# Optimization experiments

Hardware: AMD Instinct MI355X
Metric: run time of the kernel (lower is better)

Reference implementation:

```python
import jax, jax.numpy as jnp
import numpy as np

K_ATTRS = 16  # fixed number of attribute clusters (torch.unique made static for jit)
NEG_INF = jnp.float32(-1e9)


def setup_inputs() -> dict:
    key = jax.random.key(0)
    ks = jax.random.split(key, 20)
    B, T, V, D, H = 4096, 200, 100000, 64, 64
    M0, M1 = 256, 128
    FC_IN = D + D + H + D  # 256
    s = 0.02
    f32 = jnp.float32
    inp = {
        "item_id": jax.random.randint(ks[0], (B,), 0, V),
        "hist_item_ids": jax.random.randint(ks[1], (B, T), 0, V),
        "hist_item_attributes": jax.random.randint(ks[2], (B, T), 0, K_ATTRS),
        "emb_table": s * jax.random.normal(ks[3], (V, D), dtype=f32),
        "au_W1": s * jax.random.normal(ks[4], (4 * D, H), dtype=f32),
        "au_b1": jnp.zeros((H,), f32),
        "au_W2": s * jax.random.normal(ks[5], (H, 1), dtype=f32),
        "au_b2": jnp.zeros((1,), f32),
        "gru_Wx": s * jax.random.normal(ks[6], (D, 3 * H), dtype=f32),
        "gru_Wh": s * jax.random.normal(ks[7], (H, 3 * H), dtype=f32),
        "gru_b": jnp.zeros((3 * H,), f32),
        "fc_W0": s * jax.random.normal(ks[8], (FC_IN, M0), dtype=f32),
        "fc_b0": jnp.zeros((M0,), f32),
        "fc_W1": s * jax.random.normal(ks[9], (M0, M1), dtype=f32),
        "fc_b1": jnp.zeros((M1,), f32),
        "final_W": s * jax.random.normal(ks[10], (M1, 1), dtype=f32),
        "final_b": jnp.zeros((1,), f32),
    }
    return inp


def reference(item_id, hist_item_ids, hist_item_attributes, emb_table,
              au_W1, au_b1, au_W2, au_b2, gru_Wx, gru_Wh, gru_b,
              fc_W0, fc_b0, fc_W1, fc_b1, final_W, final_b):
    item = emb_table[item_id]            # [B,D]
    hist = emb_table[hist_item_ids]      # [B,T,D]
    B = item.shape[0]
    H = gru_Wh.shape[0]

    # --- DIEN: GRU over history, final hidden state ---
    xp = hist @ gru_Wx + gru_b           # [B,T,3H]

    def step(h, x):
        gz, gr, gn = jnp.split(h @ gru_Wh, 3, axis=-1)
        xz, xr, xn = jnp.split(x, 3, axis=-1)
        z = jax.nn.sigmoid(xz + gz)
        r = jax.nn.sigmoid(xr + gr)
        n = jnp.tanh(xn + r * gn)
        return (1.0 - z) * n + z * h, None

    h0 = jnp.zeros((B, H), hist.dtype)
    interest_evolution, _ = jax.lax.scan(step, h0, jnp.swapaxes(xp, 0, 1))  # [B,H]

    # --- DIN-style activation unit: score each key against the target item ---
    def act_unit(q, keys):  # q:[B,D], keys:[B,N,D] -> [B,N,1]
        qe = jnp.broadcast_to(q[:, None, :], keys.shape)
        feat = jnp.concatenate([keys, qe, keys - qe, keys * qe], axis=-1)
        hid = jax.nn.relu(feat @ au_W1 + au_b1)
        return hid @ au_W2 + au_b2

    w1 = act_unit(item, hist)                    # [B,T,1]
    user_interest_l1 = jnp.sum(w1 * hist, axis=1)  # [B,D]

    # --- attribute_group: per-attribute masked softmax + weighted sum ---
    mask = hist_item_attributes[..., None] == jnp.arange(K_ATTRS)  # [B,T,K]
    logits = jnp.where(mask, w1, NEG_INF)        # [B,T,K]
    probs = jax.nn.softmax(logits, axis=1) * mask
    cluster = jnp.einsum('btk,btd->bkd', probs, hist)  # [B,K,D]

    w2 = act_unit(item, cluster)                 # [B,K,1]
    user_interest_l2 = jnp.sum(w2 * cluster, axis=1)  # [B,D]

    combined = jnp.concatenate(
        [user_interest_l1, user_interest_l2, interest_evolution, item], axis=1)
    x = jax.nn.relu(combined @ fc_W0 + fc_b0)
    x = jax.nn.relu(x @ fc_W1 + fc_b1)
    out = x @ final_W + final_b                  # [B,1]
    return jax.nn.sigmoid(out[:, 0])             # [B]
```

## Files before the change

### kernel.cpp

```cpp
#include <hip/hip_runtime.h>
#include <hip/hip_bf16.h>

#define B_   4096
#define T_   200
#define KA   16

#define OFF_BG  0
#define OFF_WQ  4096
#define OFF_QP  (OFF_BG  + B_*T_)
#define OFF_UI1 (OFF_QP  + B_*64)
#define OFF_UI2 (OFF_UI1 + B_*64)
#define OFF_HF  (OFF_UI2 + B_*64)
#define OFF_CL  (OFF_HF  + B_*64)

typedef __attribute__((ext_vector_type(8))) short bf16x8;
typedef __attribute__((ext_vector_type(4))) float f32x4;

__device__ __forceinline__ float sigmoidf_(float x) {
  return 1.f / (1.f + __expf(-x));
}
__device__ __forceinline__ float sigf(float x) {
  return __builtin_amdgcn_rcpf(1.f + __builtin_amdgcn_exp2f(-1.44269504f * x));
}
__device__ __forceinline__ float tanhfast(float y) {
  return 1.f - 2.f * __builtin_amdgcn_rcpf(1.f + __builtin_amdgcn_exp2f(2.88539008f * y));
}
__device__ __forceinline__ short f2bf(float x) {
  unsigned u = __float_as_uint(x);
  unsigned r = (u + 0x7fffu + ((u >> 16) & 1u)) >> 16;
  return (short)r;
}
__device__ __forceinline__ unsigned cvtpk(float lo, float hi) {
  unsigned r;
  asm("v_cvt_pk_bf16_f32 %0, %1, %2" : "=v"(r) : "v"(lo), "v"(hi));
  return r;
}
union BF8 { bf16x8 v; unsigned u[4]; };

__device__ __forceinline__ bf16x8 pack8(float4 f0, float4 f1) {
  BF8 a;
  a.u[0] = cvtpk(f0.x, f0.y);
  a.u[1] = cvtpk(f0.z, f0.w);
  a.u[2] = cvtpk(f1.x, f1.y);
  a.u[3] = cvtpk(f1.z, f1.w);
  return a.v;
}
__device__ __forceinline__ bf16x8 pack8m(float4 f0, float4 f1,
                                         float4 q0, float4 q1) {
  BF8 a;
  a.u[0] = cvtpk(f0.x*q0.x, f0.y*q0.y);
  a.u[1] = cvtpk(f0.z*q0.z, f0.w*q0.w);
  a.u[2] = cvtpk(f1.x*q1.x, f1.y*q1.y);
  a.u[3] = cvtpk(f1.z*q1.z, f1.w*q1.w);
  return a.v;
}


__global__ __launch_bounds__(256) void k_prep(
    const float* __restrict__ auW1, short* __restrict__ bg,
    float* __restrict__ wq)
{
  const int i = blockIdx.x*256 + threadIdx.x;
  if (i < 8192) {
    const int k = i >> 6, col = i & 63;
    float v;
    if (k < 64) v = auW1[k*64 + col] + auW1[2*4096 + k*64 + col];
    else        v = auW1[3*4096 + (k-64)*64 + col];
    bg[((k >> 5)*4 + ((k >> 3) & 3))*512 + col*8 + (k & 7)] = f2bf(v);
  } else if (i < 12288) {
    const int j = i - 8192;
    wq[j] = auW1[(64 + (j >> 6))*64 + (j & 63)]
          - auW1[(128 + (j >> 6))*64 + (j & 63)];
  }
}

__global__ __launch_bounds__(256) void k_act1(
    const int* __restrict__ item_id, const int* __restrict__ hist_ids,
    const int* __restrict__ attrs,
    const float* __restrict__ emb, const float* __restrict__ aub1,
    const float* __restrict__ auW2, const float* __restrict__ aub2,
    const short* __restrict__ bg_in, const float* __restrict__ wq_in,
    float* __restrict__ qp_out, float* __restrict__ ui1_out,
    float* __restrict__ cluster_out)
{
  __shared__ __align__(16) char sPool[16384];
  __shared__ float sW1[208];
  __shared__ float sP[200];
  __shared__ float sM[KA], sE[KA];
  __shared__ float sItem[64], sQp[64];
  __shared__ float sQpP[4][64];
  __shared__ float sUi[4][64];
  __shared__ int   sIds[200], sAttr[200];

  short* sB2 = (short*)sPool;
  float (*sAcc)[KA][64] = (float (*)[KA][64])sPool;

  const int b = blockIdx.x;
  const int tid = threadIdx.x;
  const int wave = tid >> 6, lane = tid & 63;
  const int g = lane >> 4;
  const int c15 = lane & 15;
  const int itrow = item_id[b];

  for (int i = tid; i < 4096; i += 256)
    ((unsigned*)sB2)[i] = ((const unsigned*)bg_in)[i];
  if (tid < 64) sItem[tid] = emb[(size_t)itrow*64 + tid];
  if (tid < T_) {
    sIds[tid]  = hist_ids[(size_t)b*T_ + tid];
    sAttr[tid] = attrs[(size_t)b*T_ + tid];
  }
  __syncthreads();

  {
    const int j = tid & 63, iq = tid >> 6;
    float acc = 0.f;
    #pragma unroll
    for (int ii = 0; ii < 16; ++ii) {
      const int i = iq*16 + ii;
      acc += sItem[i] * wq_in[i*64 + j];
    }
    sQpP[iq][j] = acc;
  }
  __syncthreads();
  if (tid < 64) {
    float q = aub1[tid] + sQpP[0][tid] + sQpP[1][tid] + sQpP[2][tid] + sQpP[3][tid];
    sQp[tid] = q;
    qp_out[(size_t)b*64 + tid] = q;
  }
  __syncthreads();

  const float4* itemp = (const float4*)(emb + (size_t)itrow*64);
  float4 q0 = itemp[g*2],     q1 = itemp[g*2 + 1];
  float4 q2 = itemp[8 + g*2], q3 = itemp[8 + g*2 + 1];

  bf16x8 bfr[4][4];
  #pragma unroll
  for (int kk = 0; kk < 4; ++kk) {
    #pragma unroll
    for (int n = 0; n < 4; ++n)
      bfr[kk][n] = *(const bf16x8*)&sB2[(kk*4 + g)*512 + (n*16 + c15)*8];
  }
  float w2v[4], qpv[4];
  #pragma unroll
  for (int n = 0; n < 4; ++n) {
    w2v[n] = auW2[n*16 + c15];
    qpv[n] = sQp[n*16 + c15];
  }
  const float b2v = aub2[0];
  __syncthreads();

  for (int i = tid; i < 4*KA*64; i += 256) ((float*)sAcc)[i] = 0.f;

  for (int tt = wave; tt < 13; tt += 4) {
    const int t = tt*16 + c15;
    float4 k0{0,0,0,0}, k1{0,0,0,0}, k2{0,0,0,0}, k3{0,0,0,0};
    if (t < T_) {
      const float4* kp = (const float4*)(emb + (size_t)sIds[t]*64);
      k0 = kp[g*2];     k1 = kp[g*2 + 1];
      k2 = kp[8 + g*2]; k3 = kp[8 + g*2 + 1];
    }
    bf16x8 a0 = pack8(k0, k1);
    bf16x8 a1 = pack8(k2, k3);
    bf16x8 a2 = pack8m(k0, k1, q0, q1);
    bf16x8 a3 = pack8m(k2, k3, q2, q3);

    f32x4 acc[4];
    #pragma unroll
    for (int n = 0; n < 4; ++n) acc[n] = f32x4{qpv[n], qpv[n], qpv[n], qpv[n]};
    #pragma unroll
    for (int n = 0; n < 4; ++n) {
      acc[n] = __builtin_amdgcn_mfma_f32_16x16x32_bf16(a0, bfr[0][n], acc[n], 0, 0, 0);
      acc[n] = __builtin_amdgcn_mfma_f32_16x16x32_bf16(a1, bfr[1][n], acc[n], 0, 0, 0);
      acc[n] = __builtin_amdgcn_mfma_f32_16x16x32_bf16(a2, bfr[2][n], acc[n], 0, 0, 0);
      acc[n] = __builtin_amdgcn_mfma_f32_16x16x32_bf16(a3, bfr[3][n], acc[n], 0, 0, 0);
    }
    float ws[4] = {0.f, 0.f, 0.f, 0.f};
    #pragma unroll
    for (int n = 0; n < 4; ++n) {
      #pragma unroll
      for (int r = 0; r < 4; ++r)
        ws[r] += fmaxf(acc[n][r], 0.f) * w2v[n];
    }
    #pragma unroll
    for (int r = 0; r < 4; ++r) {
      ws[r] += __shfl_xor(ws[r], 1);
      ws[r] += __shfl_xor(ws[r], 2);
      ws[r] += __shfl_xor(ws[r], 4);
      ws[r] += __shfl_xor(ws[r], 8);
      ws[r] += b2v;
    }
    if (c15 == 0) {
      #pragma unroll
      for (int r = 0; r < 4; ++r) {
        const int trow = tt*16 + g*4 + r;
        if (trow < T_) sW1[trow] = ws[r];
      }
    }
  }
  __syncthreads();

  for (int k = wave; k < KA; k += 4) {
    float m = -1e9f;
    for (int tt4 = 0; tt4 < 4; ++tt4) {
      int t = tt4*64 + lane;
      if (t < T_ && sAttr[t] == k) m = fmaxf(m, sW1[t]);
    }
    #pragma unroll
    for (int off = 32; off > 0; off >>= 1) m = fmaxf(m, __shfl_xor(m, off));
    float e = 0.f;
    for (int tt4 = 0; tt4 < 4; ++tt4) {
      int t = tt4*64 + lane;
      if (t < T_ && sAttr[t] == k) e += __expf(sW1[t] - m);
    }
    #pragma unroll
    for (int off = 32; off > 0; off >>= 1) e += __shfl_xor(e, off);
    if (lane == 0) { sM[k] = m; sE[k] = e; }
  }
  __syncthreads();
  if (tid < T_) {
    int k = sAttr[tid];
    float e = sE[k];
    sP[tid] = (e > 0.f) ? __expf(sW1[tid] - sM[k]) * __builtin_amdgcn_rcpf(e) : 0.f;
  }
  __syncthreads();

  float uiacc = 0.f;
  {
    float vcur = emb[(size_t)sIds[wave]*64 + lane];
    for (int t = wave; t < T_; t += 4) {
      const int tn = t + 4;
      float vnext = 0.f;
      if (tn < T_) vnext = emb[(size_t)sIds[tn]*64 + lane];
      const int k = sAttr[t];
      sAcc[wave][k][lane] += sP[t] * vcur;
      uiacc += sW1[t] * vcur;
      vcur = vnext;
    }
  }
  sUi[wave][lane] = uiacc;
  __syncthreads();

  for (int i = tid; i < KA*64; i += 256) {
    cluster_out[(size_t)b*(KA*64) + i] =
        sAcc[0][0][i] + sAcc[1][0][i] + sAcc[2][0][i] + sAcc[3][0][i];
  }
  if (tid < 64) {
    ui1_out[(size_t)b*64 + tid] =
        sUi[0][tid] + sUi[1][tid] + sUi[2][tid] + sUi[3][tid];
  }
}

#define GRU_ROWS 16
__global__ __launch_bounds__(512) void k_gru(
    const int* __restrict__ hist_ids, const float* __restrict__ emb,
    const float* __restrict__ Wx, const float* __restrict__ Wh,
    const float* __restrict__ gb, float* __restrict__ hfin_out)
{
  __shared__ short sH[2][16*64];
  __shared__ short sX[4][16*64];
  __shared__ int   sIds[16*200];

  const int tid  = threadIdx.x;
  const int w    = tid >> 6;
  const int lane = tid & 63;
  const int g    = lane >> 4;
  const int c15  = lane & 15;
  const int b0   = blockIdx.x * GRU_ROWS;

  for (int i = tid; i < 16*200; i += 512) {
    const int r = i / 200, t = i - r*200;
    sIds[i] = hist_ids[(size_t)(b0 + r)*T_ + t];
  }
  for (int i = tid; i < 16*64; i += 512) sH[0][i] = 0;
  __syncthreads();

  if (w >= 4) {
    const int stane = (w - 4)*64 + lane;
    const int srow  = stane >> 4;
    const int scol  = (stane & 15) * 4;
    const int sidx  = srow*64 + (((scol >> 3) ^ (srow & 7))*8) + (scol & 7);
    const int* idrow = &sIds[srow*200];
    #pragma unroll
    for (int p = 0; p < 2; ++p) {
      const float4 f = *(const float4*)(emb + (size_t)idrow[p]*64 + scol);
      uint2 u; u.x = cvtpk(f.x, f.y); u.y = cvtpk(f.z, f.w);
      *(uint2*)&sX[p][sidx] = u;
    }
    __syncthreads();
    for (int t = 0; t < T_; ++t) {
      const int t2 = (t + 2 < T_) ? (t + 2) : (T_ - 1);
      const float4 f = *(const float4*)(emb + (size_t)idrow[t2]*64 + scol);
      uint2 u; u.x = cvtpk(f.x, f.y); u.y = cvtpk(f.z, f.w);
      *(uint2*)&sX[(t + 2) & 3][sidx] = u;
      __syncthreads();
    }
  } else {
    bf16x8 bx[3][2], bh[3][2];
    #pragma unroll
    for (int l = 0; l < 3; ++l) {
      const int jb = (l*4 + w)*16 + c15;
      #pragma unroll
      for (int kk = 0; kk < 2; ++kk) {
        bf16x8 vx, vh;
        #pragma unroll
        for (int e = 0; e < 8; ++e) {
          const int krow = kk*32 + g*8 + e;
          vx[e] = f2bf(Wx[(size_t)krow*192 + jb]);
          vh[e] = f2bf(Wh[(size_t)krow*192 + jb]);
        }
        bx[l][kk] = vx; bh[l][kk] = vh;
      }
    }
    float bias[3];
    #pragma unroll
    for (int l = 0; l < 3; ++l) bias[l] = gb[l*64 + w*16 + c15];

    const int rs = c15 & 7;
    const int ridx0 = c15*64 + ((g    ) ^ rs)*8;
    const int ridx1 = c15*64 + ((g + 4) ^ rs)*8;
    int widx[4];
    {
      const int unit = w*2 + (c15 >> 3);
      #pragma unroll
      for (int r = 0; r < 4; ++r) {
        const int row = g*4 + r;
        widx[r] = row*64 + ((unit ^ (row & 7))*8) + (c15 & 7);
      }
    }
    float hold[4] = {0.f, 0.f, 0.f, 0.f};
    __syncthreads();

    #pragma unroll 2
    for (int t = 0; t < T_; ++t) {
      const short* hbuf = sH[t & 1];
      short*       hnxt = sH[(t & 1) ^ 1];
      const short* xbuf = sX[t & 3];

      bf16x8 ax0 = *(const bf16x8*)&xbuf[ridx0];
      bf16x8 ax1 = *(const bf16x8*)&xbuf[ridx1];
      bf16x8 ah0 = *(const bf16x8*)&hbuf[ridx0];
      bf16x8 ah1 = *(const bf16x8*)&hbuf[ridx1];

      f32x4 aX[3], aH[3];
      #pragma unroll
      for (int l = 0; l < 3; ++l) {
        aX[l] = f32x4{bias[l], bias[l], bias[l], bias[l]};
        aH[l] = f32x4{0.f, 0.f, 0.f, 0.f};
      }
      #pragma unroll
      for (int l = 0; l < 3; ++l) {
        aH[l] = __builtin_amdgcn_mfma_f32_16x16x32_bf16(ah0, bh[l][0], aH[l], 0, 0, 0);
        aH[l] = __builtin_amdgcn_mfma_f32_16x16x32_bf16(ah1, bh[l][1], aH[l], 0, 0, 0);
        aX[l] = __builtin_amdgcn_mfma_f32_16x16x32_bf16(ax0, bx[l][0], aX[l], 0, 0, 0);
        aX[l] = __builtin_amdgcn_mfma_f32_16x16x32_bf16(ax1, bx[l][1], aX[l], 0, 0, 0);
      }

      #pragma unroll
      for (int r = 0; r < 4; ++r) {
        float z  = sigf(aX[0][r] + aH[0][r]);
        float rr = sigf(aX[1][r] + aH[1][r]);
        float nn = tanhfast(aX[2][r] + rr * aH[2][r]);
        hold[r] = nn + z * (hold[r] - nn);
        hnxt[widx[r]] = f2bf(hold[r]);
      }
      __syncthreads();
    }

    #pragma unroll
    for (int r = 0; r < 4; ++r)
      hfin_out[(size_t)(b0 + g*4 + r)*64 + w*16 + c15] = hold[r];
  }
}

__global__ __launch_bounds__(256) void k_act2(
    const int* __restrict__ item_id, const float* __restrict__ emb,
    const float* __restrict__ auW2, const float* __restrict__ aub2,
    const float* __restrict__ qp_in, const float* __restrict__ cluster_in,
    const short* __restrict__ bg_in, float* __restrict__ ui2_out)
{
  __shared__ short sB2[8192];
  __shared__ float sWs[4][16];
  __shared__ float sWf[16];
  __shared__ float sUi[4][64];

  const int b = blockIdx.x;
  const int tid = threadIdx.x;
  const int wave = tid >> 6, lane = tid & 63;
  const int g = lane >> 4;
  const int c15 = lane & 15;
  const int itrow = item_id[b];

  for (int i = tid; i < 4096; i += 256)
    ((unsigned*)sB2)[i] = ((const unsigned*)bg_in)[i];
  __syncthreads();

  const float4* itemp = (const float4*)(emb + (size_t)itrow*64);
  float4 q0 = itemp[g*2],     q1 = itemp[g*2 + 1];
  float4 q2 = itemp[8 + g*2], q3 = itemp[8 + g*2 + 1];
  const float4* kp = (const float4*)(cluster_in + (size_t)b*(KA*64) + c15*64);
  float4 k0 = kp[g*2],     k1 = kp[g*2 + 1];
  float4 k2 = kp[8 + g*2], k3 = kp[8 + g*2 + 1];
  bf16x8 a0 = pack8(k0, k1);
  bf16x8 a1 = pack8(k2, k3);
  bf16x8 a2 = pack8m(k0, k1, q0, q1);
  bf16x8 a3 = pack8m(k2, k3, q2, q3);

  const float qpv = qp_in[(size_t)b*64 + wave*16 + c15];
  const float w2v = auW2[wave*16 + c15];
  f32x4 acc = f32x4{qpv, qpv, qpv, qpv};
  acc = __builtin_amdgcn_mfma_f32_16x16x32_bf16(a0, *(const bf16x8*)&sB2[(0*4+g)*512 + (wave*16+c15)*8], acc, 0, 0, 0);
  acc = __builtin_amdgcn_mfma_f32_16x16x32_bf16(a1, *(const bf16x8*)&sB2[(1*4+g)*512 + (wave*16+c15)*8], acc, 0, 0, 0);
  acc = __builtin_amdgcn_mfma_f32_16x16x32_bf16(a2, *(const bf16x8*)&sB2[(2*4+g)*512 + (wave*16+c15)*8], acc, 0, 0, 0);
  acc = __builtin_amdgcn_mfma_f32_16x16x32_bf16(a3, *(const bf16x8*)&sB2[(3*4+g)*512 + (wave*16+c15)*8], acc, 0, 0, 0);

  float ws[4];
  #pragma unroll
  for (int r = 0; r < 4; ++r) {
    float v = fmaxf(acc[r], 0.f) * w2v;
    v += __shfl_xor(v, 1);
    v += __shfl_xor(v, 2);
    v += __shfl_xor(v, 4);
    v += __shfl_xor(v, 8);
    ws[r] = v;
  }
  if (c15 == 0) {
    #pragma unroll
    for (int r = 0; r < 4; ++r) sWs[wave][g*4 + r] = ws[r];
  }
  __syncthreads();
  if (tid < KA)
    sWf[tid] = sWs[0][tid] + sWs[1][tid] + sWs[2][tid] + sWs[3][tid] + aub2[0];
  __syncthreads();

  float uiacc = 0.f;
  #pragma unroll
  for (int kk = 0; kk < 4; ++kk) {
    const int k = wave*4 + kk;
    uiacc += sWf[k] * cluster_in[(size_t)b*(KA*64) + k*64 + lane];
  }
  sUi[wave][lane] = uiacc;
  __syncthreads();
  if (tid < 64) {
    ui2_out[(size_t)b*64 + tid] =
        sUi[0][tid] + sUi[1][tid] + sUi[2][tid] + sUi[3][tid];
  }
}

#define MLP_ROWS 16
__global__ __launch_bounds__(256) void k_mlp(
    const int* __restrict__ item_id, const float* __restrict__ emb,
    const float* __restrict__ ui1, const float* __restrict__ ui2,
    const float* __restrict__ hfin,
    const float* __restrict__ W0, const float* __restrict__ b0,
    const float* __restrict__ W1, const float* __restrict__ b1,
    const float* __restrict__ fW, const float* __restrict__ fb,
    float* __restrict__ out)
{
  __shared__ float sC[MLP_ROWS][256];
  __shared__ float sX0[MLP_ROWS][256];
  __shared__ float sX1[MLP_ROWS][128];
  const int tid = threadIdx.x;
  const int rb  = blockIdx.x * MLP_ROWS;

  for (int idx = tid; idx < MLP_ROWS*256; idx += 256) {
    int r = idx >> 8, c = idx & 255;
    size_t row = (size_t)(rb + r);
    float v;
    if (c < 64)       v = ui1[row*64 + c];
    else if (c < 128) v = ui2[row*64 + (c-64)];
    else if (c < 192) v = hfin[row*64 + (c-128)];
    else              v = emb[(size_t)item_id[row]*64 + (c-192)];
    sC[r][c] = v;
  }
  __syncthreads();
  {
    float acc[MLP_ROWS];
    #pragma unroll
    for (int r = 0; r < MLP_ROWS; ++r) acc[r] = b0[tid];
    #pragma unroll 4
    for (int i = 0; i < 256; ++i) {
      float w = W0[(size_t)i*256 + tid];
      #pragma unroll
      for (int r = 0; r < MLP_ROWS; ++r) acc[r] += sC[r][i] * w;
    }
    #pragma unroll
    for (int r = 0; r < MLP_ROWS; ++r) sX0[r][tid] = fmaxf(acc[r], 0.f);
  }
  __syncthreads();
  if (tid < 128) {
    float acc[MLP_ROWS];
    #pragma unroll
    for (int r = 0; r < MLP_ROWS; ++r) acc[r] = b1[tid];
    #pragma unroll 4
    for (int i = 0; i < 256; ++i) {
      float w = W1[(size_t)i*128 + tid];
      #pragma unroll
      for (int r = 0; r < MLP_ROWS; ++r) acc[r] += sX0[r][i] * w;
    }
    #pragma unroll
    for (int r = 0; r < MLP_ROWS; ++r) sX1[r][tid] = fmaxf(acc[r], 0.f);
  }
  __syncthreads();
  {
    int r = tid >> 4, l16 = tid & 15;
    float p = 0.f;
    for (int i = l16; i < 128; i += 16) p += sX1[r][i] * fW[i];
    #pragma unroll
    for (int off = 8; off > 0; off >>= 1) p += __shfl_xor(p, off);
    if (l16 == 0) {
      float logit = p + fb[0];
      out[rb + r] = sigmoidf_(logit);
    }
  }
}

extern "C" void kernel_launch(void* const* d_in, const int* in_sizes, int n_in,
                              void* d_out, int out_size, void* d_ws, size_t ws_size,
                              hipStream_t stream)
{
  const int*   item_id  = (const int*)d_in[0];
  const int*   hist_ids = (const int*)d_in[1];
  const int*   attrs    = (const int*)d_in[2];
  const float* emb      = (const float*)d_in[3];
  const float* auW1     = (const float*)d_in[4];
  const float* aub1     = (const float*)d_in[5];
  const float* auW2     = (const float*)d_in[6];
  const float* aub2     = (const float*)d_in[7];
  const float* gWx      = (const float*)d_in[8];
  const float* gWh      = (const float*)d_in[9];
  const float* gb       = (const float*)d_in[10];
  const float* W0       = (const float*)d_in[11];
  const float* b0       = (const float*)d_in[12];
  const float* W1       = (const float*)d_in[13];
  const float* b1       = (const float*)d_in[14];
  const float* fW       = (const float*)d_in[15];
  const float* fb       = (const float*)d_in[16];

  float* out = (float*)d_out;
  float* ws  = (float*)d_ws;
  short* bg      = (short*)(ws + OFF_BG);
  float* wq      = ws + OFF_WQ;
  float* qp      = ws + OFF_QP;
  float* ui1     = ws + OFF_UI1;
  float* ui2     = ws + OFF_UI2;
  float* hfin    = ws + OFF_HF;
  float* cluster = ws + OFF_CL;

  k_prep<<<48, 256, 0, stream>>>(auW1, bg, wq);
  k_act1<<<B_, 256, 0, stream>>>(item_id, hist_ids, attrs, emb, aub1,
                                 auW2, aub2, bg, wq, qp, ui1, cluster);
  k_gru<<<B_/GRU_ROWS, 512, 0, stream>>>(hist_ids, emb, gWx, gWh, gb, hfin);
  k_act2<<<B_, 256, 0, stream>>>(item_id, emb, auW2, aub2, qp, cluster, bg,
                                 ui2);
  k_mlp<<<B_/MLP_ROWS, 256, 0, stream>>>(item_id, emb, ui1, ui2, hfin,
                                         W0, b0, W1, b1, fW, fb, out);
}
```

Before: 324.6 us.

## Stage bf16 history rows in LDS and compute cluster sums from them

The act1 kernel now writes the bf16-packed history embeddings into a swizzled LDS buffer during the MFMA scoring pass. It then reuses that buffer for the per-attribute cluster sums and the l1 interest sum, replacing a second global gather of the fp32 embeddings. Each wave now owns four attribute clusters in registers instead of doing shared-memory atomic-like accumulation plus a 4-way reduction. The scoring loop also prefetches the next tile's rows. The trade-off is bf16 precision for the weighted sums, and each wave now loops over all 200 timesteps.

After: 408.7 us. 25.9% more time.

```diff
diff --git a/kernel.cpp b/kernel.cpp
--- a/kernel.cpp
+++ b/kernel.cpp
@@ -29,6 +29,9 @@
   unsigned u = __float_as_uint(x);
   unsigned r = (u + 0x7fffu + ((u >> 16) & 1u)) >> 16;
   return (short)r;
+}
+__device__ __forceinline__ float bf2f(unsigned short h) {
+  return __uint_as_float((unsigned)h << 16);
 }
 __device__ __forceinline__ unsigned cvtpk(float lo, float hi) {
   unsigned r;
@@ -83,7 +86,7 @@
     float* __restrict__ qp_out, float* __restrict__ ui1_out,
     float* __restrict__ cluster_out)
 {
-  __shared__ __align__(16) char sPool[16384];
+  __shared__ __align__(16) short sKp[13*1024];
   __shared__ float sW1[208];
   __shared__ float sP[200];
   __shared__ float sM[KA], sE[KA];
@@ -92,9 +95,6 @@
   __shared__ float sUi[4][64];
   __shared__ int   sIds[200], sAttr[200];
 
-  short* sB2 = (short*)sPool;
-  float (*sAcc)[KA][64] = (float (*)[KA][64])sPool;
-
   const int b = blockIdx.x;
   const int tid = threadIdx.x;
   const int wave = tid >> 6, lane = tid & 63;
@@ -103,7 +103,7 @@
   const int itrow = item_id[b];
 
   for (int i = tid; i < 4096; i += 256)
-    ((unsigned*)sB2)[i] = ((const unsigned*)bg_in)[i];
+    ((unsigned*)sKp)[i] = ((const unsigned*)bg_in)[i];
   if (tid < 64) sItem[tid] = emb[(size_t)itrow*64 + tid];
   if (tid < T_) {
     sIds[tid]  = hist_ids[(size_t)b*T_ + tid];
@@ -138,7 +138,7 @@
   for (int kk = 0; kk < 4; ++kk) {
     #pragma unroll
     for (int n = 0; n < 4; ++n)
-      bfr[kk][n] = *(const bf16x8*)&sB2[(kk*4 + g)*512 + (n*16 + c15)*8];
+      bfr[kk][n] = *(const bf16x8*)&sKp[(kk*4 + g)*512 + (n*16 + c15)*8];
   }
   float w2v[4], qpv[4];
   #pragma unroll
@@ -149,52 +149,68 @@
   const float b2v = aub2[0];
   __syncthreads();
 
-  for (int i = tid; i < 4*KA*64; i += 256) ((float*)sAcc)[i] = 0.f;
-
-  for (int tt = wave; tt < 13; tt += 4) {
-    const int t = tt*16 + c15;
-    float4 k0{0,0,0,0}, k1{0,0,0,0}, k2{0,0,0,0}, k3{0,0,0,0};
-    if (t < T_) {
-      const float4* kp = (const float4*)(emb + (size_t)sIds[t]*64);
-      k0 = kp[g*2];     k1 = kp[g*2 + 1];
-      k2 = kp[8 + g*2]; k3 = kp[8 + g*2 + 1];
-    }
-    bf16x8 a0 = pack8(k0, k1);
-    bf16x8 a1 = pack8(k2, k3);
-    bf16x8 a2 = pack8m(k0, k1, q0, q1);
-    bf16x8 a3 = pack8m(k2, k3, q2, q3);
-
-    f32x4 acc[4];
-    #pragma unroll
-    for (int n = 0; n < 4; ++n) acc[n] = f32x4{qpv[n], qpv[n], qpv[n], qpv[n]};
-    #pragma unroll
-    for (int n = 0; n < 4; ++n) {
-      acc[n] = __builtin_amdgcn_mfma_f32_16x16x32_bf16(a0, bfr[0][n], acc[n], 0, 0, 0);
-      acc[n] = __builtin_amdgcn_mfma_f32_16x16x32_bf16(a1, bfr[1][n], acc[n], 0, 0, 0);
-      acc[n] = __builtin_amdgcn_mfma_f32_16x16x32_bf16(a2, bfr[2][n], acc[n], 0, 0, 0);
-      acc[n] = __builtin_amdgcn_mfma_f32_16x16x32_bf16(a3, bfr[3][n], acc[n], 0, 0, 0);
-    }
-    float ws[4] = {0.f, 0.f, 0.f, 0.f};
-    #pragma unroll
-    for (int n = 0; n < 4; ++n) {
-      #pragma unroll
-      for (int r = 0; r < 4; ++r)
-        ws[r] += fmaxf(acc[n][r], 0.f) * w2v[n];
-    }
-    #pragma unroll
-    for (int r = 0; r < 4; ++r) {
-      ws[r] += __shfl_xor(ws[r], 1);
-      ws[r] += __shfl_xor(ws[r], 2);
-      ws[r] += __shfl_xor(ws[r], 4);
-      ws[r] += __shfl_xor(ws[r], 8);
-      ws[r] += b2v;
-    }
-    if (c15 == 0) {
+  const int rsw = c15 & 7;
+  {
+    float4 c0, c1, c2, c3;
+    {
+      const int t = wave*16 + c15;
+      const int tc = (t < T_) ? t : (T_ - 1);
+      const float4* kp = (const float4*)(emb + (size_t)sIds[tc]*64);
+      c0 = kp[g*2];     c1 = kp[g*2 + 1];
+      c2 = kp[8 + g*2]; c3 = kp[8 + g*2 + 1];
+    }
+    for (int tt = wave; tt < 13; tt += 4) {
+      float4 n0{0,0,0,0}, n1{0,0,0,0}, n2{0,0,0,0}, n3{0,0,0,0};
+      const int ttn = tt + 4;
+      if (ttn < 13) {
+        const int t = ttn*16 + c15;
+        const int tc = (t < T_) ? t : (T_ - 1);
+        const float4* kp = (const float4*)(emb + (size_t)sIds[tc]*64);
+        n0 = kp[g*2];     n1 = kp[g*2 + 1];
+        n2 = kp[8 + g*2]; n3 = kp[8 + g*2 + 1];
+      }
+
+      bf16x8 a0 = pack8(c0, c1);
+      bf16x8 a1 = pack8(c2, c3);
+      bf16x8 a2 = pack8m(c0, c1, q0, q1);
+      bf16x8 a3 = pack8m(c2, c3, q2, q3);
+
+      *(bf16x8*)&sKp[tt*1024 + c15*64 + ((g       ^ rsw)*8)] = a0;
+      *(bf16x8*)&sKp[tt*1024 + c15*64 + (((g + 4) ^ rsw)*8)] = a1;
+
+      f32x4 acc[4];
+      #pragma unroll
+      for (int n = 0; n < 4; ++n) acc[n] = f32x4{qpv[n], qpv[n], qpv[n], qpv[n]};
+      #pragma unroll
+      for (int n = 0; n < 4; ++n) {
+        acc[n] = __builtin_amdgcn_mfma_f32_16x16x32_bf16(a0, bfr[0][n], acc[n], 0, 0, 0);
+        acc[n] = __builtin_amdgcn_mfma_f32_16x16x32_bf16(a1, bfr[1][n], acc[n], 0, 0, 0);
+        acc[n] = __builtin_amdgcn_mfma_f32_16x16x32_bf16(a2, bfr[2][n], acc[n], 0, 0, 0);
+        acc[n] = __builtin_amdgcn_mfma_f32_16x16x32_bf16(a3, bfr[3][n], acc[n], 0, 0, 0);
+      }
+      float ws[4] = {0.f, 0.f, 0.f, 0.f};
+      #pragma unroll
+      for (int n = 0; n < 4; ++n) {
+        #pragma unroll
+        for (int r = 0; r < 4; ++r)
+          ws[r] += fmaxf(acc[n][r], 0.f) * w2v[n];
+      }
       #pragma unroll
       for (int r = 0; r < 4; ++r) {
-        const int trow = tt*16 + g*4 + r;
-        if (trow < T_) sW1[trow] = ws[r];
-      }
+        ws[r] += __shfl_xor(ws[r], 1);
+        ws[r] += __shfl_xor(ws[r], 2);
+        ws[r] += __shfl_xor(ws[r], 4);
+        ws[r] += __shfl_xor(ws[r], 8);
+        ws[r] += b2v;
+      }
+      if (c15 == 0) {
+        #pragma unroll
+        for (int r = 0; r < 4; ++r) {
+          const int trow = tt*16 + g*4 + r;
+          if (trow < T_) sW1[trow] = ws[r];
+        }
+      }
+      c0 = n0; c1 = n1; c2 = n2; c3 = n3;
     }
   }
   __syncthreads();
@@ -224,26 +240,31 @@
   }
   __syncthreads();
 
-  float uiacc = 0.f;
   {
-    float vcur = emb[(size_t)sIds[wave]*64 + lane];
-    for (int t = wave; t < T_; t += 4) {
-      const int tn = t + 4;
-      float vnext = 0.f;
-      if (tn < T_) vnext = emb[(size_t)sIds[tn]*64 + lane];
-      const int k = sAttr[t];
-      sAcc[wave][k][lane] += sP[t] * vcur;
-      uiacc += sW1[t] * vcur;
-      vcur = vnext;
-    }
-  }
-  sUi[wave][lane] = uiacc;
-  __syncthreads();
-
-  for (int i = tid; i < KA*64; i += 256) {
-    cluster_out[(size_t)b*(KA*64) + i] =
-        sAcc[0][0][i] + sAcc[1][0][i] + sAcc[2][0][i] + sAcc[3][0][i];
-  }
+    float acc0 = 0.f, acc1 = 0.f, acc2 = 0.f, acc3 = 0.f, uiacc = 0.f;
+    const int kbase = wave*4;
+    const int u = lane >> 3, e7 = lane & 7;
+    for (int t = 0; t < T_; ++t) {
+      const int tr = t & 15;
+      const unsigned short hv =
+          ((const unsigned short*)sKp)[(t >> 4)*1024 + tr*64 + ((u ^ (tr & 7))*8) + e7];
+      const float v = bf2f(hv);
+      const float p = sP[t];
+      const int kk = sAttr[t] - kbase;
+      acc0 += ((kk == 0) ? p : 0.f) * v;
+      acc1 += ((kk == 1) ? p : 0.f) * v;
+      acc2 += ((kk == 2) ? p : 0.f) * v;
+      acc3 += ((kk == 3) ? p : 0.f) * v;
+      uiacc += (((t & 3) == wave) ? sW1[t] : 0.f) * v;
+    }
+    float* crow = cluster_out + (size_t)b*(KA*64) + kbase*64 + lane;
+    crow[0]   = acc0;
+    crow[64]  = acc1;
+    crow[128] = acc2;
+    crow[192] = acc3;
+    sUi[wave][lane] = uiacc;
+  }
+  __syncthreads();
   if (tid < 64) {
     ui1_out[(size_t)b*64 + tid] =
         sUi[0][tid] + sUi[1][tid] + sUi[2][tid] + sUi[3][tid];
```

## Stage history embeddings once in LDS as bf16 and reuse across act1 phases

Applied to the files above, without the earlier changes.

k_act1 now gathers each block's 200 history embedding rows from global memory once, converts them to bf16, and stores them in a swizzled LDS buffer. Both the MFMA attention scoring and the later weighted-sum pass read from that buffer instead of gathering from global twice. The block grows to 512 threads, and the cluster accumulation and the ui1 sum are split across separate wave groups. This removes a duplicate random gather over the embedding table. In exchange the l1 and cluster sums now use bf16-rounded values, which costs some accuracy, and the added LDS use may lower occupancy.

Result: slower. 348.5 us (+7.4%).

```diff
diff --git a/kernel.cpp b/kernel.cpp
--- a/kernel.cpp
+++ b/kernel.cpp
@@ -29,6 +29,9 @@
   unsigned u = __float_as_uint(x);
   unsigned r = (u + 0x7fffu + ((u >> 16) & 1u)) >> 16;
   return (short)r;
+}
+__device__ __forceinline__ float bf2f(unsigned short h) {
+  return __uint_as_float((unsigned)h << 16);
 }
 __device__ __forceinline__ unsigned cvtpk(float lo, float hi) {
   unsigned r;
@@ -53,6 +56,18 @@
   a.u[2] = cvtpk(f1.x*q1.x, f1.y*q1.y);
   a.u[3] = cvtpk(f1.z*q1.z, f1.w*q1.w);
   return a.v;
+}
+__device__ __forceinline__ bf16x8 mulq8(bf16x8 a, float4 qa, float4 qb) {
+  BF8 in; in.v = a; BF8 o;
+  float l0 = __uint_as_float(in.u[0] << 16), h0 = __uint_as_float(in.u[0] & 0xffff0000u);
+  float l1 = __uint_as_float(in.u[1] << 16), h1 = __uint_as_float(in.u[1] & 0xffff0000u);
+  float l2 = __uint_as_float(in.u[2] << 16), h2 = __uint_as_float(in.u[2] & 0xffff0000u);
+  float l3 = __uint_as_float(in.u[3] << 16), h3 = __uint_as_float(in.u[3] & 0xffff0000u);
+  o.u[0] = cvtpk(l0*qa.x, h0*qa.y);
+  o.u[1] = cvtpk(l1*qa.z, h1*qa.w);
+  o.u[2] = cvtpk(l2*qb.x, h2*qb.y);
+  o.u[3] = cvtpk(l3*qb.z, h3*qb.w);
+  return o.v;
 }
 
 
@@ -74,7 +89,7 @@
   }
 }
 
-__global__ __launch_bounds__(256) void k_act1(
+__global__ __launch_bounds__(512) void k_act1(
     const int* __restrict__ item_id, const int* __restrict__ hist_ids,
     const int* __restrict__ attrs,
     const float* __restrict__ emb, const float* __restrict__ aub1,
@@ -84,25 +99,27 @@
     float* __restrict__ cluster_out)
 {
   __shared__ __align__(16) char sPool[16384];
+  __shared__ __align__(16) unsigned sRows[208*32];
   __shared__ float sW1[208];
   __shared__ float sP[200];
   __shared__ float sM[KA], sE[KA];
   __shared__ float sItem[64], sQp[64];
-  __shared__ float sQpP[4][64];
+  __shared__ float sQpP[8][64];
   __shared__ float sUi[4][64];
   __shared__ int   sIds[200], sAttr[200];
 
   short* sB2 = (short*)sPool;
   float (*sAcc)[KA][64] = (float (*)[KA][64])sPool;
+  const unsigned short* rowsU = (const unsigned short*)sRows;
 
   const int b = blockIdx.x;
   const int tid = threadIdx.x;
-  const int wave = tid >> 6, lane = tid & 63;
+  const int w = tid >> 6, lane = tid & 63;
   const int g = lane >> 4;
   const int c15 = lane & 15;
   const int itrow = item_id[b];
 
-  for (int i = tid; i < 4096; i += 256)
+  for (int i = tid; i < 4096; i += 512)
     ((unsigned*)sB2)[i] = ((const unsigned*)bg_in)[i];
   if (tid < 64) sItem[tid] = emb[(size_t)itrow*64 + tid];
   if (tid < T_) {
@@ -111,19 +128,33 @@
   }
   __syncthreads();
 
+  #pragma unroll
+  for (int it = 0; it < 13; ++it) {
+    const int i = it*512 + tid;
+    const int r = i >> 5, dw = i & 31;
+    unsigned val = 0;
+    if (r < T_) {
+      const float2 f = *(const float2*)(emb + (size_t)sIds[r]*64 + dw*2);
+      val = cvtpk(f.x, f.y);
+    }
+    sRows[r*32 + (dw ^ ((r & 7) << 2))] = val;
+  }
   {
     const int j = tid & 63, iq = tid >> 6;
     float acc = 0.f;
     #pragma unroll
-    for (int ii = 0; ii < 16; ++ii) {
-      const int i = iq*16 + ii;
+    for (int ii = 0; ii < 8; ++ii) {
+      const int i = iq*8 + ii;
       acc += sItem[i] * wq_in[i*64 + j];
     }
     sQpP[iq][j] = acc;
   }
   __syncthreads();
+
   if (tid < 64) {
-    float q = aub1[tid] + sQpP[0][tid] + sQpP[1][tid] + sQpP[2][tid] + sQpP[3][tid];
+    float q = aub1[tid];
+    #pragma unroll
+    for (int iq = 0; iq < 8; ++iq) q += sQpP[iq][tid];
     sQp[tid] = q;
     qp_out[(size_t)b*64 + tid] = q;
   }
@@ -149,20 +180,14 @@
   const float b2v = aub2[0];
   __syncthreads();
 
-  for (int i = tid; i < 4*KA*64; i += 256) ((float*)sAcc)[i] = 0.f;
-
-  for (int tt = wave; tt < 13; tt += 4) {
+  for (int i = tid; i < 4*KA*64; i += 512) ((float*)sAcc)[i] = 0.f;
+
+  for (int tt = w; tt < 13; tt += 8) {
     const int t = tt*16 + c15;
-    float4 k0{0,0,0,0}, k1{0,0,0,0}, k2{0,0,0,0}, k3{0,0,0,0};
-    if (t < T_) {
-      const float4* kp = (const float4*)(emb + (size_t)sIds[t]*64);
-      k0 = kp[g*2];     k1 = kp[g*2 + 1];
-      k2 = kp[8 + g*2]; k3 = kp[8 + g*2 + 1];
-    }
-    bf16x8 a0 = pack8(k0, k1);
-    bf16x8 a1 = pack8(k2, k3);
-    bf16x8 a2 = pack8m(k0, k1, q0, q1);
-    bf16x8 a3 = pack8m(k2, k3, q2, q3);
+    bf16x8 a0 = *(const bf16x8*)&rowsU[t*64 + (((g    ) ^ (t & 7)) << 3)];
+    bf16x8 a1 = *(const bf16x8*)&rowsU[t*64 + (((g + 4) ^ (t & 7)) << 3)];
+    bf16x8 a2 = mulq8(a0, q0, q1);
+    bf16x8 a3 = mulq8(a1, q2, q3);
 
     f32x4 acc[4];
     #pragma unroll
@@ -199,7 +224,7 @@
   }
   __syncthreads();
 
-  for (int k = wave; k < KA; k += 4) {
+  for (int k = w; k < KA; k += 8) {
     float m = -1e9f;
     for (int tt4 = 0; tt4 < 4; ++tt4) {
       int t = tt4*64 + lane;
@@ -224,23 +249,22 @@
   }
   __syncthreads();
 
-  float uiacc = 0.f;
-  {
-    float vcur = emb[(size_t)sIds[wave]*64 + lane];
-    for (int t = wave; t < T_; t += 4) {
-      const int tn = t + 4;
-      float vnext = 0.f;
-      if (tn < T_) vnext = emb[(size_t)sIds[tn]*64 + lane];
-      const int k = sAttr[t];
-      sAcc[wave][k][lane] += sP[t] * vcur;
-      uiacc += sW1[t] * vcur;
-      vcur = vnext;
-    }
-  }
-  sUi[wave][lane] = uiacc;
-  __syncthreads();
-
-  for (int i = tid; i < KA*64; i += 256) {
+  if (w < 4) {
+    for (int t = w; t < T_; t += 4) {
+      const float v = bf2f(rowsU[t*64 + (lane ^ ((t & 7) << 3))]);
+      sAcc[w][sAttr[t]][lane] += sP[t] * v;
+    }
+  } else {
+    float uiacc = 0.f;
+    for (int t = w - 4; t < T_; t += 4) {
+      const float v = bf2f(rowsU[t*64 + (lane ^ ((t & 7) << 3))]);
+      uiacc += sW1[t] * v;
+    }
+    sUi[w - 4][lane] = uiacc;
+  }
+  __syncthreads();
+
+  for (int i = tid; i < KA*64; i += 512) {
     cluster_out[(size_t)b*(KA*64) + i] =
         sAcc[0][0][i] + sAcc[1][0][i] + sAcc[2][0][i] + sAcc[3][0][i];
   }
@@ -547,7 +571,7 @@
   float* cluster = ws + OFF_CL;
 
   k_prep<<<48, 256, 0, stream>>>(auW1, bg, wq);
-  k_act1<<<B_, 256, 0, stream>>>(item_id, hist_ids, attrs, emb, aub1,
+  k_act1<<<B_, 512, 0, stream>>>(item_id, hist_ids, attrs, emb, aub1,
                                  auW2, aub2, bg, wq, qp, ui1, cluster);
   k_gru<<<B_/GRU_ROWS, 512, 0, stream>>>(hist_ids, emb, gWx, gWh, gb, hfin);
   k_act2<<<B_, 256, 0, stream>>>(item_id, emb, auW2, aub2, qp, cluster, bg,
```
